# Performance work log

Measured on AMD Instinct MI355X. Metric: run time of the kernel, lower is better.

## Reference

```python
import jax, jax.numpy as jnp
import numpy as np

TOKENS, IN_F, OUT_F = 8192, 4096, 4096
MAXQ = 15          # 4-bit
ZERO_POINT = 8     # (maxq + 1) // 2


def _make_24_mask(key, in_f, out_f):
    """Boolean 2:4 mask: exactly 2 True per contiguous group of 4 along in_f."""
    scores = jax.random.normal(key, (in_f // 4, 4, out_f), dtype=jnp.float32)
    # ascending sort along the group-of-4 axis; index 2 = 2nd largest value
    thresh = jnp.sort(scores, axis=1)[:, 2:3, :]
    mask = scores >= thresh  # keeps top-2 of each group of 4
    return mask.reshape(in_f, out_f)


def setup_inputs() -> dict:
    key = jax.random.key(0)
    k_x, k_q, k_m, k_s = jax.random.split(key, 4)
    x = jax.random.normal(k_x, (TOKENS, IN_F), dtype=jnp.float16)
    qvals = jax.random.randint(k_q, (IN_F, OUT_F), 0, MAXQ + 1, dtype=jnp.int32)
    mask = _make_24_mask(k_m, IN_F, OUT_F)
    # per-column scales (groupsize == infeatures -> one scale row)
    scales = (jax.random.uniform(k_s, (1, OUT_F), dtype=jnp.float32) * 0.01 + 0.001).astype(jnp.float16)
    return {"x": x, "qvals": qvals, "mask": mask, "scales": scales}


def reference(x, qvals, mask, scales):
    # Dequantize: W = (q - zero_point) * scale, then apply 2:4 sparsity mask.
    w = (qvals.astype(jnp.float32) - ZERO_POINT) * scales.astype(jnp.float32)  # [in, out]
    w = jnp.where(mask, w, 0.0).astype(x.dtype)
    # GEMM with fp32 accumulation (as the fused kernel does), output in x.dtype
    y = jnp.einsum("ti,io->to", x, w, preferred_element_type=jnp.float32)
    return y.astype(x.dtype)
```

## Files before the change

### kernel.cpp

```cpp
#include <hip/hip_runtime.h>
#include <stdint.h>

typedef short short8 __attribute__((ext_vector_type(8)));
typedef float floatx4 __attribute__((ext_vector_type(4)));

#define M_TOK 8192
#define K_IN  4096
#define N_OUT 4096
#define NTT   (K_IN / 32)

static __device__ __forceinline__ float bf2f(ushort u) {
    union { uint32_t u; float f; } v;
    v.u = ((uint32_t)u) << 16;
    return v.f;
}
static __device__ __forceinline__ ushort f2bf(float f) {
    union { float f; uint32_t u; } v;
    v.f = f;
    uint32_t u = v.u;
    uint32_t r = (u + 0x7FFFu + ((u >> 16) & 1u)) >> 16;
    return (ushort)r;
}

__global__ void detect_zero_kernel(int* __restrict__ flags) {
    if (threadIdx.x < 3) flags[1 + threadIdx.x] = 0;
}

__global__ __launch_bounds__(256) void detect_count_kernel(
    const unsigned char* __restrict__ mb, int* __restrict__ flags) {
    const ushort* mh = (const ushort*)mb;
    const unsigned int* mw = (const unsigned int*)mb;
    __shared__ int sh[3];
    if (threadIdx.x < 3) sh[threadIdx.x] = 0;
    __syncthreads();
    int s = blockIdx.x * 256 + threadIdx.x;
    int grp = s & 255;
    int o   = (s * 97) & 4095;
    int c1 = 0, c2 = 0, c4 = 0;
    #pragma unroll
    for (int r = 0; r < 4; ++r) {
        size_t idx = (size_t)(4 * grp + r) * N_OUT + o;
        c1 += (mb[idx] != 0);
        c2 += (mh[idx] != 0);
        c4 += (mw[idx] != 0);
    }
    if (c1 != 2) atomicAdd(&sh[0], 1);
    if (c2 != 2) atomicAdd(&sh[1], 1);
    if (c4 != 2) atomicAdd(&sh[2], 1);
    __syncthreads();
    if (threadIdx.x == 0) {
        atomicAdd(&flags[1], sh[0]);
        atomicAdd(&flags[2], sh[1]);
        atomicAdd(&flags[3], sh[2]);
    }
}

__global__ void detect_final_kernel(int* __restrict__ flags) {
    if (threadIdx.x == 0) {
        int size = 4, best = flags[3];
        if (flags[2] < best) { size = 2; best = flags[2]; }
        if (flags[1] < best) { size = 1; }
        flags[0] = size;
    }
}

__global__ __launch_bounds__(256) void convert_x_kernel(
    const float* __restrict__ xf, ushort* __restrict__ Xb) {
    const int total = M_TOK * K_IN;
    const int stride = gridDim.x * 256 * 8;
    for (int i = (blockIdx.x * 256 + threadIdx.x) * 8; i < total; i += stride) {
        floatx4 f0 = *(const floatx4*)&xf[i];
        floatx4 f1 = *(const floatx4*)&xf[i + 4];
        short8 v;
        #pragma unroll
        for (int j = 0; j < 4; ++j) v[j]     = (short)f2bf(f0[j]);
        #pragma unroll
        for (int j = 0; j < 4; ++j) v[4 + j] = (short)f2bf(f1[j]);
        *(short8*)&Xb[i] = v;
    }
}

__global__ __launch_bounds__(256) void dequant_kernel(
    const int* __restrict__ q, const void* __restrict__ maskp,
    const float* __restrict__ scales, ushort* __restrict__ Bt,
    const int* __restrict__ flagp) {
    const int msize = flagp[0];
    const int i0 = blockIdx.x * 64;
    const int o0 = blockIdx.y * 64;
    const int tid = threadIdx.x;
    const unsigned char* mb = (const unsigned char*)maskp;
    const ushort* mh = (const ushort*)maskp;
    const unsigned int* mi = (const unsigned int*)maskp;
    __shared__ ushort T[64][72];

    for (int p = 0; p < 16; ++p) {
        int idx = p * 256 + tid;
        int r = idx >> 6, c = idx & 63;
        size_t gi = (size_t)(i0 + r) * N_OUT + (o0 + c);
        bool m;
        if (msize == 1)      m = (mb[gi] != 0);
        else if (msize == 2) m = (mh[gi] != 0);
        else                 m = (mi[gi] != 0);
        float s = scales[o0 + c];
        float w = m ? (float)(q[gi] - 8) * s : 0.0f;
        T[r][c] = f2bf(w);
    }
    __syncthreads();
    for (int p = 0; p < 2; ++p) {
        int ol = p * 32 + (tid >> 3);
        int i8 = (tid & 7) * 8;
        short8 v;
        #pragma unroll
        for (int j = 0; j < 8; ++j) v[j] = (short)T[i8 + j][ol];
        *(short8*)&Bt[(size_t)(o0 + ol) * K_IN + i0 + i8] = v;
    }
}

#define GL2L16(gp, lbase)                                                      \
    __builtin_amdgcn_global_load_lds(                                          \
        (const __attribute__((address_space(1))) void*)(gp),                   \
        (__attribute__((address_space(3))) void*)(lbase), 16, 0, 0)

#define MFMA16(a, b, c) __builtin_amdgcn_mfma_f32_16x16x32_bf16(a, b, c, 0, 0, 0)

__global__ __launch_bounds__(512, 2) void gemm_kernel(
    const ushort* __restrict__ X,
    const ushort* __restrict__ Bt,
    float* __restrict__ Y) {
    __shared__ ushort As[4][256][32];
    __shared__ ushort Bs[4][256][32];

    const int tid  = threadIdx.x;
    const int w    = tid >> 6;
    const int lane = tid & 63;

    const int r    = blockIdx.x >> 8;
    const int kb   = blockIdx.x & 255;
    const int xcd  = kb & 7;
    const int j    = kb >> 3;
    const int m_tile = r * 16 + (xcd & 1) * 8 + (j & 7);
    const int n_tile = (xcd >> 1) * 4 + (j >> 3);
    const int row0 = m_tile * 256;
    const int col0 = n_tile * 256;
    const int wm = w >> 2, wn = w & 3;

    floatx4 acc[8][4] = {};

    const int srow   = (w << 4) + (lane >> 2);
    const int schunk = (lane & 3) ^ ((lane >> 3) & 3);
    const ushort* gA = X  + (size_t)(row0 + srow) * K_IN + schunk * 8;
    const ushort* gB = Bt + (size_t)(col0 + srow) * K_IN + schunk * 8;

    const int fr = lane & 15, g = lane >> 4;
    const int fsw = (fr >> 1) & 3;

    #define STGU(gbase, arr, SL, tt)                                           \
        do {                                                                   \
            GL2L16(gbase + (size_t)(tt) * 32,                                  \
                   (char*)&arr[SL][w * 16][0] + lane * 16);                    \
            GL2L16(gbase + (size_t)128 * K_IN + (size_t)(tt) * 32,             \
                   (char*)&arr[SL][128 + w * 16][0] + lane * 16);              \
        } while (0)

    #define TILE1(SL, T)                                                       \
        do {                                                                   \
            const bool sg = (T) + 3 < NTT;                                     \
            short8 afr[8], bfr[4];                                             \
            _Pragma("unroll")                                                  \
            for (int n = 0; n < 4; ++n)                                        \
                bfr[n] = *(const short8*)&Bs[SL][wn * 64 + n * 16 + fr]        \
                             [(g ^ fsw) * 8];                                  \
            _Pragma("unroll")                                                  \
            for (int m = 0; m < 8; ++m)                                        \
                afr[m] = *(const short8*)&As[SL][wm * 128 + m * 16 + fr]       \
                             [(g ^ fsw) * 8];                                  \
            if (sg) {                                                          \
                STGU(gA, As, ((SL) + 3) & 3, (T) + 3);                         \
                STGU(gB, Bs, ((SL) + 3) & 3, (T) + 3);                         \
            }                                                                  \
            __builtin_amdgcn_s_barrier();                                      \
            asm volatile("s_waitcnt lgkmcnt(0)" ::: "memory");                 \
            __builtin_amdgcn_sched_barrier(0);                                 \
            __builtin_amdgcn_s_setprio(1);                                     \
            _Pragma("unroll")                                                  \
            for (int m = 0; m < 8; ++m)                                        \
                _Pragma("unroll")                                              \
                for (int n = 0; n < 4; ++n)                                    \
                    acc[m][n] = MFMA16(afr[m], bfr[n], acc[m][n]);             \
            __builtin_amdgcn_s_setprio(0);                                     \
            if (sg)                 { asm volatile("s_waitcnt vmcnt(8)" ::: "memory"); } \
            else if ((T) + 2 < NTT) { asm volatile("s_waitcnt vmcnt(4)" ::: "memory"); } \
            else                    { asm volatile("s_waitcnt vmcnt(0)" ::: "memory"); } \
            __builtin_amdgcn_s_barrier();                                      \
        } while (0)

    STGU(gA, As, 0, 0); STGU(gB, Bs, 0, 0);
    STGU(gA, As, 1, 1); STGU(gB, Bs, 1, 1);
    STGU(gA, As, 2, 2); STGU(gB, Bs, 2, 2);
    asm volatile("s_waitcnt vmcnt(8)" ::: "memory");
    __builtin_amdgcn_s_barrier();

    for (int t4 = 0; t4 < NTT / 4; ++t4) {
        const int T = t4 * 4;
        TILE1(0, T);
        TILE1(1, T + 1);
        TILE1(2, T + 2);
        TILE1(3, T + 3);
    }

    const int fq = lane >> 4;
    #pragma unroll
    for (int m = 0; m < 8; ++m)
        #pragma unroll
        for (int n = 0; n < 4; ++n)
            #pragma unroll
            for (int i = 0; i < 4; ++i) {
                int rr = row0 + wm * 128 + m * 16 + fq * 4 + i;
                int cc = col0 + wn * 64 + n * 16 + fr;
                Y[(size_t)rr * N_OUT + cc] = acc[m][n][i];
            }
    #undef TILE1
    #undef STGU
}

__global__ __launch_bounds__(256) void fallback_kernel(
    const float* __restrict__ xf, const int* __restrict__ q,
    const void* __restrict__ maskp, const float* __restrict__ scales,
    float* __restrict__ Y, const int* __restrict__ flagp) {
    const int msize = flagp[0];
    const int o = blockIdx.x * 256 + threadIdx.x;
    const int t = blockIdx.y;
    const unsigned char* mb = (const unsigned char*)maskp;
    const ushort* mh = (const ushort*)maskp;
    const unsigned int* mi = (const unsigned int*)maskp;
    float s = scales[o];
    float acc = 0.f;
    for (int i = 0; i < K_IN; ++i) {
        float x = bf2f(f2bf(xf[(size_t)t * K_IN + i]));
        size_t gi = (size_t)i * N_OUT + o;
        bool m;
        if (msize == 1)      m = (mb[gi] != 0);
        else if (msize == 2) m = (mh[gi] != 0);
        else                 m = (mi[gi] != 0);
        if (m) acc += x * bf2f(f2bf((float)(q[gi] - 8) * s));
    }
    Y[(size_t)t * N_OUT + o] = acc;
}

extern "C" void kernel_launch(void* const* d_in, const int* in_sizes, int n_in,
                              void* d_out, int out_size, void* d_ws, size_t ws_size,
                              hipStream_t stream) {
    const float* x      = (const float*)d_in[0];
    const int*   q      = (const int*)d_in[1];
    const void*  mask   = d_in[2];
    const float* scales = (const float*)d_in[3];
    float* y = (float*)d_out;

    const size_t BT_OFF = 64;
    const size_t XB_OFF = BT_OFF + (size_t)N_OUT * K_IN * 2;
    const size_t need   = XB_OFF + (size_t)M_TOK * K_IN * 2;

    int* flags = (int*)d_ws;
    detect_zero_kernel<<<1, 64, 0, stream>>>(flags);
    detect_count_kernel<<<64, 256, 0, stream>>>(
        (const unsigned char*)mask, flags);
    detect_final_kernel<<<1, 64, 0, stream>>>(flags);

    if (ws_size >= need) {
        ushort* Bt = (ushort*)((char*)d_ws + BT_OFF);
        ushort* Xb = (ushort*)((char*)d_ws + XB_OFF);
        convert_x_kernel<<<4096, 256, 0, stream>>>(x, Xb);
        dequant_kernel<<<dim3(K_IN / 64, N_OUT / 64), 256, 0, stream>>>(
            q, mask, scales, Bt, flags);
        gemm_kernel<<<dim3((M_TOK / 256) * (N_OUT / 256)), 512, 0, stream>>>(
            Xb, Bt, y);
    } else {
        fallback_kernel<<<dim3(N_OUT / 256, M_TOK), 256, 0, stream>>>(
            x, q, mask, scales, y, flags);
    }
}
```

Baseline: 363.9 us.

## Shrink GEMM block to 128x256 tile with 256 threads and double buffering

Restructures the GEMM from a 256x256 tile with 512 threads and a 4-stage LDS ring into a 128x256 tile with 256 threads and a 2-stage double buffer. The block-to-tile swizzle is updated for the larger grid. Each wave now covers all 128 rows against a 64-column slice. LDS use drops from 128KB to 48KB, which may allow more resident blocks. In exchange, each K step ends with a full vmcnt(0) wait, so there is less prefetch depth to hide global latency, and arithmetic intensity per block is lower.

```diff
diff --git a/kernel.cpp b/kernel.cpp
--- a/kernel.cpp
+++ b/kernel.cpp
@@ -123,61 +123,61 @@
 
 #define MFMA16(a, b, c) __builtin_amdgcn_mfma_f32_16x16x32_bf16(a, b, c, 0, 0, 0)
 
-__global__ __launch_bounds__(512, 2) void gemm_kernel(
+__global__ __launch_bounds__(256, 2) void gemm_kernel(
     const ushort* __restrict__ X,
     const ushort* __restrict__ Bt,
     float* __restrict__ Y) {
-    __shared__ ushort As[4][256][32];
-    __shared__ ushort Bs[4][256][32];
+    __shared__ ushort As[2][128][32];
+    __shared__ ushort Bs[2][256][32];
 
     const int tid  = threadIdx.x;
     const int w    = tid >> 6;
     const int lane = tid & 63;
 
-    const int r    = blockIdx.x >> 8;
-    const int kb   = blockIdx.x & 255;
-    const int xcd  = kb & 7;
-    const int j    = kb >> 3;
-    const int m_tile = r * 16 + (xcd & 1) * 8 + (j & 7);
-    const int n_tile = (xcd >> 1) * 4 + (j >> 3);
-    const int row0 = m_tile * 256;
+    const int xcd = blockIdx.x & 7;
+    const int jj  = (blockIdx.x >> 3) & 63;
+    const int rr0 = blockIdx.x >> 9;
+    const int m_tile = rr0 * 32 + (xcd & 1) * 16 + (jj & 15);
+    const int n_tile = (xcd >> 1) * 4 + (jj >> 4);
+    const int row0 = m_tile * 128;
     const int col0 = n_tile * 256;
-    const int wm = w >> 2, wn = w & 3;
 
     floatx4 acc[8][4] = {};
 
-    const int srow   = (w << 4) + (lane >> 2);
-    const int schunk = (lane & 3) ^ ((lane >> 3) & 3);
-    const ushort* gA = X  + (size_t)(row0 + srow) * K_IN + schunk * 8;
-    const ushort* gB = Bt + (size_t)(col0 + srow) * K_IN + schunk * 8;
+    const int schunk = (tid & 3) ^ ((tid >> 3) & 3);
+    const ushort* gA = X  + (size_t)(row0 + (tid >> 2)) * K_IN + schunk * 8;
+    const ushort* gB = Bt + (size_t)(col0 + (tid >> 2)) * K_IN + schunk * 8;
 
     const int fr = lane & 15, g = lane >> 4;
     const int fsw = (fr >> 1) & 3;
 
-    #define STGU(gbase, arr, SL, tt)                                           \
+    #define STG(BF, tt)                                                        \
         do {                                                                   \
-            GL2L16(gbase + (size_t)(tt) * 32,                                  \
-                   (char*)&arr[SL][w * 16][0] + lane * 16);                    \
-            GL2L16(gbase + (size_t)128 * K_IN + (size_t)(tt) * 32,             \
-                   (char*)&arr[SL][128 + w * 16][0] + lane * 16);              \
+            GL2L16(gA + (size_t)(tt) * 32,                                     \
+                   (char*)&As[BF][w * 16][0] + lane * 16);                     \
+            GL2L16(gA + (size_t)64 * K_IN + (size_t)(tt) * 32,                 \
+                   (char*)&As[BF][64 + w * 16][0] + lane * 16);                \
+            GL2L16(gB + (size_t)(tt) * 32,                                     \
+                   (char*)&Bs[BF][w * 16][0] + lane * 16);                     \
+            GL2L16(gB + (size_t)64 * K_IN + (size_t)(tt) * 32,                 \
+                   (char*)&Bs[BF][64 + w * 16][0] + lane * 16);                \
+            GL2L16(gB + (size_t)128 * K_IN + (size_t)(tt) * 32,                \
+                   (char*)&Bs[BF][128 + w * 16][0] + lane * 16);               \
+            GL2L16(gB + (size_t)192 * K_IN + (size_t)(tt) * 32,                \
+                   (char*)&Bs[BF][192 + w * 16][0] + lane * 16);               \
         } while (0)
 
-    #define TILE1(SL, T)                                                       \
+    #define TILE(BF, T)                                                        \
         do {                                                                   \
-            const bool sg = (T) + 3 < NTT;                                     \
             short8 afr[8], bfr[4];                                             \
             _Pragma("unroll")                                                  \
             for (int n = 0; n < 4; ++n)                                        \
-                bfr[n] = *(const short8*)&Bs[SL][wn * 64 + n * 16 + fr]        \
+                bfr[n] = *(const short8*)&Bs[BF][w * 64 + n * 16 + fr]         \
                              [(g ^ fsw) * 8];                                  \
             _Pragma("unroll")                                                  \
             for (int m = 0; m < 8; ++m)                                        \
-                afr[m] = *(const short8*)&As[SL][wm * 128 + m * 16 + fr]       \
-                             [(g ^ fsw) * 8];                                  \
-            if (sg) {                                                          \
-                STGU(gA, As, ((SL) + 3) & 3, (T) + 3);                         \
-                STGU(gB, Bs, ((SL) + 3) & 3, (T) + 3);                         \
-            }                                                                  \
+                afr[m] = *(const short8*)&As[BF][m * 16 + fr][(g ^ fsw) * 8];  \
+            if ((T) + 1 < NTT) STG((BF) ^ 1, (T) + 1);                         \
             __builtin_amdgcn_s_barrier();                                      \
             asm volatile("s_waitcnt lgkmcnt(0)" ::: "memory");                 \
             __builtin_amdgcn_sched_barrier(0);                                 \
@@ -188,24 +188,17 @@
                 for (int n = 0; n < 4; ++n)                                    \
                     acc[m][n] = MFMA16(afr[m], bfr[n], acc[m][n]);             \
             __builtin_amdgcn_s_setprio(0);                                     \
-            if (sg)                 { asm volatile("s_waitcnt vmcnt(8)" ::: "memory"); } \
-            else if ((T) + 2 < NTT) { asm volatile("s_waitcnt vmcnt(4)" ::: "memory"); } \
-            else                    { asm volatile("s_waitcnt vmcnt(0)" ::: "memory"); } \
+            asm volatile("s_waitcnt vmcnt(0)" ::: "memory");                   \
             __builtin_amdgcn_s_barrier();                                      \
         } while (0)
 
-    STGU(gA, As, 0, 0); STGU(gB, Bs, 0, 0);
-    STGU(gA, As, 1, 1); STGU(gB, Bs, 1, 1);
-    STGU(gA, As, 2, 2); STGU(gB, Bs, 2, 2);
-    asm volatile("s_waitcnt vmcnt(8)" ::: "memory");
+    STG(0, 0);
+    asm volatile("s_waitcnt vmcnt(0)" ::: "memory");
     __builtin_amdgcn_s_barrier();
 
-    for (int t4 = 0; t4 < NTT / 4; ++t4) {
-        const int T = t4 * 4;
-        TILE1(0, T);
-        TILE1(1, T + 1);
-        TILE1(2, T + 2);
-        TILE1(3, T + 3);
+    for (int t = 0; t < NTT; t += 2) {
+        TILE(0, t);
+        TILE(1, t + 1);
     }
 
     const int fq = lane >> 4;
@@ -215,12 +208,12 @@
         for (int n = 0; n < 4; ++n)
             #pragma unroll
             for (int i = 0; i < 4; ++i) {
-                int rr = row0 + wm * 128 + m * 16 + fq * 4 + i;
-                int cc = col0 + wn * 64 + n * 16 + fr;
+                int rr = row0 + m * 16 + fq * 4 + i;
+                int cc = col0 + w * 64 + n * 16 + fr;
                 Y[(size_t)rr * N_OUT + cc] = acc[m][n][i];
             }
-    #undef TILE1
-    #undef STGU
+    #undef TILE
+    #undef STG
 }
 
 __global__ __launch_bounds__(256) void fallback_kernel(
@@ -272,7 +265,7 @@
         convert_x_kernel<<<4096, 256, 0, stream>>>(x, Xb);
         dequant_kernel<<<dim3(K_IN / 64, N_OUT / 64), 256, 0, stream>>>(
             q, mask, scales, Bt, flags);
-        gemm_kernel<<<dim3((M_TOK / 256) * (N_OUT / 256)), 512, 0, stream>>>(
+        gemm_kernel<<<dim3((M_TOK / 128) * (N_OUT / 256)), 256, 0, stream>>>(
             Xb, Bt, y);
     } else {
         fallback_kernel<<<dim3(N_OUT / 256, M_TOK), 256, 0, stream>>>(
```

After: 361.6 us. About the same (-0.6%).
